# Performance work log

Measured on AMD Instinct MI355X. Metric: run time of the kernel, lower is better.

The kernel has to match this reference:

```python
import jax, jax.numpy as jnp
import numpy as np

L, B, P, D, H, DH, KV, M, S, A = 12, 8, 800, 1024, 8, 256, 1, 4096, 50, 32
ROPE_BASE = 10000.0
NEG = -1e30


def _rms(x, w):
    return (x * jax.lax.rsqrt(jnp.mean(x * x, -1, keepdims=True) + 1e-6)) * (1.0 + w)


def _rope(x, cos, sin):
    # x: [B,h,S,DH]; cos/sin: [B,1,S,DH//2]
    x1, x2 = jnp.split(x, 2, axis=-1)
    return jnp.concatenate([x1 * cos - x2 * sin, x2 * cos + x1 * sin], -1)


def setup_inputs() -> dict:
    key = jax.random.key(0)
    ks = iter(jax.random.split(key, 40))
    def nrm(shape, s=0.02):
        return jax.random.normal(next(ks), shape, jnp.float32) * s
    return {
        'prefix_pad_masks': jnp.ones((B, P), jnp.bool_),
        'x_t': jax.random.normal(next(ks), (B, S, A), jnp.float32),
        'timestep': jax.random.uniform(next(ks), (B,), jnp.float32),
        'dt': jnp.full((1,), 0.1, jnp.float32),
        'cache_k': nrm((L, B, KV, P, DH), 1.0),
        'cache_v': nrm((L, B, KV, P, DH), 1.0),
        'w_act_in': nrm((A, D)), 'b_act_in': jnp.zeros((D,), jnp.float32),
        'w_t1': nrm((D, D)), 'b_t1': jnp.zeros((D,), jnp.float32),
        'w_t2': nrm((D, D)), 'b_t2': jnp.zeros((D,), jnp.float32),
        'ln1_w': jnp.zeros((L, D), jnp.float32),
        'ada1_w': nrm((L, D, D)),
        'ln2_w': jnp.zeros((L, D), jnp.float32),
        'wq': nrm((L, D, H * DH)), 'wk': nrm((L, D, KV * DH)),
        'wv': nrm((L, D, KV * DH)), 'wo': nrm((L, H * DH, D)),
        'wg': nrm((L, D, M)), 'wu': nrm((L, D, M)), 'wd': nrm((L, M, D)),
        'lnf_w': jnp.zeros((D,), jnp.float32), 'adaf_w': nrm((D, D)),
        'w_act_out': nrm((D, A)), 'b_act_out': jnp.zeros((A,), jnp.float32),
    }


def reference(prefix_pad_masks, x_t, timestep, dt, cache_k, cache_v,
              w_act_in, b_act_in, w_t1, b_t1, w_t2, b_t2,
              ln1_w, ada1_w, ln2_w, wq, wk, wv, wo, wg, wu, wd,
              lnf_w, adaf_w, w_act_out, b_act_out):
    b, s, _ = x_t.shape
    p = prefix_pad_masks.shape[1]
    # --- embed_suffix: action projection + sinusoidal time -> MLP -> adaRMS cond ---
    suffix = x_t @ w_act_in + b_act_in                              # [B,S,D]
    half = D // 2
    freqs = jnp.exp(-jnp.log(jnp.float32(10000.0)) * jnp.arange(half, dtype=jnp.float32) / half)
    ang = timestep[:, None] * freqs[None, :]
    temb = jnp.concatenate([jnp.sin(ang), jnp.cos(ang)], -1)        # [B,D]
    cond = jax.nn.silu(temb @ w_t1 + b_t1) @ w_t2 + b_t2            # adarms_cond [B,D]
    # --- prefix-suffix 2D attention mask (make_att_2d_masks_trt) ---
    suffix_pad = jnp.ones((b, s), jnp.int32)
    suffix_att = jnp.concatenate([jnp.ones((b, 1), jnp.int32), jnp.zeros((b, s - 1), jnp.int32)], 1)
    cums = jnp.cumsum(suffix_att, 1)
    att2d = cums[:, None, :] <= cums[:, :, None]
    pad2d = (suffix_pad[:, None, :] * suffix_pad[:, :, None]).astype(bool)
    pre2d = jnp.broadcast_to(prefix_pad_masks[:, None, :], (b, s, p))
    full = jnp.concatenate([pre2d, att2d & pad2d], 2)               # [B,S,P+S]
    bias = jnp.where(full, 0.0, NEG)[:, None, :, :].astype(jnp.float32)
    # --- position ids: prefix offset + suffix cumsum - 1 ---
    offs = jnp.sum(prefix_pad_masks.astype(jnp.int32), -1)[:, None]
    pos = offs + jnp.cumsum(suffix_pad, 1) - 1                      # [B,S]
    inv = 1.0 / (ROPE_BASE ** (jnp.arange(0, DH, 2, dtype=jnp.float32) / DH))
    rang = pos[..., None].astype(jnp.float32) * inv                 # [B,S,DH/2]
    cos = jnp.cos(rang)[:, None]
    sin = jnp.sin(rang)[:, None]
    # --- gemma expert (eager attention over KV cache + suffix) ---
    h = suffix * jnp.sqrt(jnp.float32(D))
    def layer(hc, xs):
        l1, a1, l2, Wq, Wk, Wv, Wo, Wg, Wu, Wd, ck, cv = xs
        x = _rms(hc, l1) * (1.0 + (cond @ a1)[:, None, :])
        q = (x @ Wq).reshape(b, s, H, DH).transpose(0, 2, 1, 3)
        k = (x @ Wk).reshape(b, s, KV, DH).transpose(0, 2, 1, 3)
        v = (x @ Wv).reshape(b, s, KV, DH).transpose(0, 2, 1, 3)
        q = _rope(q, cos, sin)
        k = _rope(k, cos, sin)
        kf = jnp.repeat(jnp.concatenate([ck, k], 2), H // KV, 1)    # [B,H,P+S,DH]
        vf = jnp.repeat(jnp.concatenate([cv, v], 2), H // KV, 1)
        sc = jnp.einsum('bhsd,bhtd->bhst', q, kf) / jnp.sqrt(jnp.float32(DH)) + bias
        at = jax.nn.softmax(sc, -1)
        o = jnp.einsum('bhst,bhtd->bhsd', at, vf).transpose(0, 2, 1, 3).reshape(b, s, H * DH)
        hc = hc + o @ Wo
        x2 = _rms(hc, l2)
        hc = hc + (jax.nn.gelu(x2 @ Wg, approximate=True) * (x2 @ Wu)) @ Wd
        return hc, None
    h, _ = jax.lax.scan(layer, h, (ln1_w, ada1_w, ln2_w, wq, wk, wv, wo, wg, wu, wd, cache_k, cache_v))
    hf = _rms(h, lnf_w) * (1.0 + (cond @ adaf_w)[:, None, :])
    v_t = hf[:, -S:].astype(jnp.float32) @ w_act_out + b_act_out    # action_out_proj
    return x_t + dt.reshape(1, 1, 1) * v_t                          # Euler step
```

## Files before the change

kernel.cpp:

```cpp
#include <hip/hip_runtime.h>
#include <hip/hip_bf16.h>
#include <math.h>

#define NLAYER 12
#define NB 8
#define NP 800
#define ND 1024
#define NH 8
#define NDH 256
#define NM 4096
#define NS 50
#define NA 32
#define NKEYS 850
#define KPAD 896
#define CH 128

typedef unsigned short ushort_t;
typedef unsigned int u32;
using f32x4  = __attribute__((ext_vector_type(4))) float;
using short8 = __attribute__((ext_vector_type(8))) short;

__device__ __forceinline__ u32 pack_bf2(float lo, float hi) {
  u32 a = __float_as_uint(lo);
  u32 b = __float_as_uint(hi);
  a += 0x7fffu + ((a >> 16) & 1u);
  b += 0x7fffu + ((b >> 16) & 1u);
  return (a >> 16) | (b & 0xffff0000u);
}
__device__ __forceinline__ ushort_t bf1(float x) {
  u32 a = __float_as_uint(x);
  a += 0x7fffu + ((a >> 16) & 1u);
  return (ushort_t)(a >> 16);
}
__device__ __forceinline__ float ubf(ushort_t h) {
  return __uint_as_float(((u32)h) << 16);
}
__device__ __forceinline__ void async_cp16(const void* g, const void* l) {
  __builtin_amdgcn_global_load_lds(
      (const __attribute__((address_space(1))) u32*)g,
      (__attribute__((address_space(3))) u32*)l, 16, 0, 0);
}


__global__ void cvt_permute_kernel(const float* __restrict__ src, ushort_t* __restrict__ dst, long nrows) {
  long idx = (long)blockIdx.x * 256 + threadIdx.x;
  long row = idx >> 5;
  int t = (int)(idx & 31);
  if (row >= nrows) return;
  const float* s = src + row * 256 + t * 4;
  float4 lo = *reinterpret_cast<const float4*>(s);
  float4 hi = *reinterpret_cast<const float4*>(s + 128);
  ushort_t* d = dst + row * 256 + t * 8;
  *reinterpret_cast<uint4*>(d) =
      make_uint4(pack_bf2(lo.x, hi.x), pack_bf2(lo.y, hi.y),
                 pack_bf2(lo.z, hi.z), pack_bf2(lo.w, hi.w));
}

template<int MODE>
__global__ __launch_bounds__(256) void transpose_cvt(
    const float* __restrict__ src, long sz, ushort_t* __restrict__ dst, long dz,
    int R, int C, int ldd, int halfOff) {
  __shared__ float Ls[64][65];
  const float* s = src + (long)blockIdx.z * sz;
  ushort_t* d    = dst + (long)blockIdx.z * dz;
  int c0 = blockIdx.x * 64, r0 = blockIdx.y * 64;
  int t = threadIdx.x;
  int rr = t >> 4;
  int cc = (t & 15) * 4;
#pragma unroll
  for (int j = 0; j < 4; ++j) {
    int rl = rr + j * 16;
    int r = r0 + rl;
    float4 v = make_float4(0.f, 0.f, 0.f, 0.f);
    if (r < R) v = *reinterpret_cast<const float4*>(s + (long)r * C + c0 + cc);
    Ls[rl][cc] = v.x; Ls[rl][cc+1] = v.y; Ls[rl][cc+2] = v.z; Ls[rl][cc+3] = v.w;
  }
  __syncthreads();
  int dr = t >> 2;
  int rc = (t & 3) * 16;
  int cg = c0 + dr;
  long orow;
  if (MODE == 0)      orow = cg;
  else if (MODE == 1) orow = ((long)(cg >> 5) << 6) + (cg & 31) + halfOff;
  else                orow = (long)(cg & ~255) + ((cg & 127) << 1) + ((cg >> 7) & 1);
  ushort_t* drow = d + orow * ldd + r0 + rc;
#pragma unroll
  for (int i = 0; i < 16; i += 2) {
    int sr = r0 + rc + i;
    if (sr < R) {
      u32 p = pack_bf2(Ls[rc + i][dr], Ls[rc + i + 1][dr]);
      *reinterpret_cast<u32*>(drow + i) = p;
    }
  }
}


__global__ void temb_kernel(const float* __restrict__ ts, float* __restrict__ temb) {
  int idx = blockIdx.x * 256 + threadIdx.x;
  if (idx >= NB * ND) return;
  int b = idx >> 10, d = idx & 1023;
  int i = d & 511;
  float f = __expf(-logf(10000.f) * (float)i / 512.f);
  float ang = ts[b] * f;
  temb[idx] = (d < 512) ? sinf(ang) : cosf(ang);
}

__global__ void suffix_kernel(const float* __restrict__ x_t, const float* __restrict__ w,
                              const float* __restrict__ bias, float* __restrict__ h) {
  int m = blockIdx.x;
  __shared__ float xs[NA];
  if (threadIdx.x < NA) xs[threadIdx.x] = x_t[m * NA + threadIdx.x];
  __syncthreads();
  for (int n = threadIdx.x; n < ND; n += 256) {
    float acc = bias[n];
#pragma unroll
    for (int k = 0; k < NA; ++k) acc += xs[k] * w[k * ND + n];
    h[m * ND + n] = acc * 32.0f;
  }
}

__global__ void rope_table_kernel(float* __restrict__ cosT, float* __restrict__ sinT) {
  int idx = blockIdx.x * 256 + threadIdx.x;
  if (idx >= NS * 128) return;
  int s = idx >> 7, i = idx & 127;
  float inv = __expf(-(float)(2 * i) / 256.f * logf(10000.f));
  float ang = (float)(NP + s) * inv;
  cosT[idx] = cosf(ang);
  sinT[idx] = sinf(ang);
}

template<bool BFOUT>
__global__ void rms_kernel(const float* __restrict__ hin, const float* __restrict__ w,
                           const float* __restrict__ ada, void* __restrict__ outv) {
  int m = blockIdx.x;
  int b = m / NS;
  int d0 = threadIdx.x * 4;
  float4 v = *reinterpret_cast<const float4*>(hin + (long)m * ND + d0);
  float ss = v.x*v.x + v.y*v.y + v.z*v.z + v.w*v.w;
#pragma unroll
  for (int off = 32; off > 0; off >>= 1) ss += __shfl_down(ss, off);
  __shared__ float red[4];
  int lane = threadIdx.x & 63, wid = threadIdx.x >> 6;
  if (lane == 0) red[wid] = ss;
  __syncthreads();
  float tot = red[0] + red[1] + red[2] + red[3];
  float r = rsqrtf(tot * (1.f / ND) + 1e-6f);
  float4 wv = *reinterpret_cast<const float4*>(w + d0);
  float4 o;
  o.x = v.x * r * (1.f + wv.x);
  o.y = v.y * r * (1.f + wv.y);
  o.z = v.z * r * (1.f + wv.z);
  o.w = v.w * r * (1.f + wv.w);
  if (ada) {
    float4 av = *reinterpret_cast<const float4*>(ada + (long)b * ND + d0);
    o.x *= (1.f + av.x); o.y *= (1.f + av.y); o.z *= (1.f + av.z); o.w *= (1.f + av.w);
  }
  if (BFOUT) {
    *reinterpret_cast<uint2*>((ushort_t*)outv + (long)m * ND + d0) =
        make_uint2(pack_bf2(o.x, o.y), pack_bf2(o.z, o.w));
  } else {
    *reinterpret_cast<float4*>((float*)outv + (long)m * ND + d0) = o;
  }
}

__global__ void final_kernel(const float* __restrict__ hf, const float* __restrict__ w,
                             const float* __restrict__ bias, const float* __restrict__ x_t,
                             const float* __restrict__ dt, float* __restrict__ out) {
  int m = blockIdx.x;
  int a = threadIdx.x & 31;
  int kg = threadIdx.x >> 5;
  float acc = 0.f;
  for (int k = kg; k < ND; k += 8) acc += hf[(long)m * ND + k] * w[k * NA + a];
  __shared__ float red[256];
  red[threadIdx.x] = acc;
  __syncthreads();
  if (threadIdx.x < NA) {
    float s = 0.f;
#pragma unroll
    for (int g = 0; g < 8; ++g) s += red[g * 32 + a];
    out[m * NA + a] = x_t[m * NA + a] + dt[0] * (s + bias[a]);
  }
}

__global__ __launch_bounds__(256) void gemm64acc(
    const ushort_t* __restrict__ A,
    const ushort_t* __restrict__ B,
    float* __restrict__ C,
    int M, int N, int K, int lda, int ldb, int ldc, int kpb) {
  const int kbeg = blockIdx.z * kpb;
  const int kend = kbeg + kpb;

  const int m0 = blockIdx.x * 64;
  const int n0 = blockIdx.y * 64;
  const int tid = threadIdx.x;
  const int lane = tid & 63;
  const int wbase = tid & 192;
  const int wid = wbase >> 6;
  const int wm = (wid >> 1) * 32;
  const int wn = (wid & 1) * 32;
  const int l15 = lane & 15;
  const int l4  = lane >> 4;

  __shared__ ushort_t As[2][64 * 64];
  __shared__ ushort_t Bs[2][64 * 64];

  f32x4 acc[2][2] = {};

  const int ci0 = wbase + lane;
  const int row0 = ci0 >> 3;
  const int kc0 = (ci0 & 7) << 3;
  const int ci1 = 256 + ci0;
  const int row1 = ci1 >> 3;
  const int kc1 = (ci1 & 7) << 3;
  int gra0 = m0 + row0; if (gra0 > M - 1) gra0 = M - 1;
  int gra1 = m0 + row1; if (gra1 > M - 1) gra1 = M - 1;
  const int n_0 = n0 + row0;
  const int n_1 = n0 + row1;

  auto stage = [&](int buf, int k0) {
    async_cp16(A + (long)gra0 * lda + k0 + kc0, (const char*)As[buf] + ci0 * 16);
    async_cp16(B + (long)n_0 * ldb + k0 + kc0, (const char*)Bs[buf] + ci0 * 16);
    async_cp16(A + (long)gra1 * lda + k0 + kc1, (const char*)As[buf] + ci1 * 16);
    async_cp16(B + (long)n_1 * ldb + k0 + kc1, (const char*)Bs[buf] + ci1 * 16);
  };

  const int nt = (kend - kbeg) >> 6;
  stage(0, kbeg);
  __syncthreads();
  int cur = 0;
  for (int t = 0; t < nt; ++t) {
    if (t + 1 < nt) stage(cur ^ 1, kbeg + (t + 1) * 64);
    const ushort_t* Ac = As[cur];
    const ushort_t* Bc = Bs[cur];
#pragma unroll
    for (int ks = 0; ks < 2; ++ks) {
      short8 af[2], bf[2];
#pragma unroll
      for (int mi = 0; mi < 2; ++mi)
        af[mi] = *reinterpret_cast<const short8*>(&Ac[(wm + mi * 16 + l15) * 64 + ks * 32 + l4 * 8]);
#pragma unroll
      for (int ni = 0; ni < 2; ++ni)
        bf[ni] = *reinterpret_cast<const short8*>(&Bc[(wn + ni * 16 + l15) * 64 + ks * 32 + l4 * 8]);
#pragma unroll
      for (int mi = 0; mi < 2; ++mi)
#pragma unroll
        for (int ni = 0; ni < 2; ++ni)
          acc[mi][ni] = __builtin_amdgcn_mfma_f32_16x16x32_bf16(af[mi], bf[ni], acc[mi][ni], 0, 0, 0);
    }
    __syncthreads();
    cur ^= 1;
  }

#pragma unroll
  for (int mi = 0; mi < 2; ++mi) {
#pragma unroll
    for (int ni = 0; ni < 2; ++ni) {
      int col = n0 + wn + ni * 16 + l15;
      int rb  = m0 + wm + mi * 16 + l4 * 4;
      if (col >= N) continue;
#pragma unroll
      for (int r = 0; r < 4; ++r) {
        int row = rb + r;
        if (row >= M) continue;
        atomicAdd(&C[(long)row * ldc + col], acc[mi][ni][r]);
      }
    }
  }
}

__global__ __launch_bounds__(256) void gemm64rope(
    const ushort_t* __restrict__ A,
    const ushort_t* __restrict__ B,
    const float* __restrict__ cosT, const float* __restrict__ sinT,
    ushort_t* __restrict__ qTo, ushort_t* __restrict__ k_new,
    ushort_t* __restrict__ vT_l) {
  const int M = 400, K = 1024, lda = 1024, ldb = 1024;
  const int m0 = blockIdx.x * 64;
  const int n0 = blockIdx.y * 64;
  const int tid = threadIdx.x;
  const int lane = tid & 63;
  const int wbase = tid & 192;
  const int wid = wbase >> 6;
  const int wm = (wid >> 1) * 32;
  const int wn = (wid & 1) * 32;
  const int l15 = lane & 15;
  const int l4  = lane >> 4;

  __shared__ ushort_t As[2][64 * 64];
  __shared__ ushort_t Bs[2][64 * 64];

  f32x4 acc[2][2] = {};

  const int ci0 = wbase + lane;
  const int row0 = ci0 >> 3;
  const int kc0 = (ci0 & 7) << 3;
  const int ci1 = 256 + ci0;
  const int row1 = ci1 >> 3;
  const int kc1 = (ci1 & 7) << 3;
  int gra0 = m0 + row0; if (gra0 > M - 1) gra0 = M - 1;
  int gra1 = m0 + row1; if (gra1 > M - 1) gra1 = M - 1;
  const int n_0 = n0 + row0;
  const int n_1 = n0 + row1;

  auto stage = [&](int buf, int k0) {
    async_cp16(A + (long)gra0 * lda + k0 + kc0, (const char*)As[buf] + ci0 * 16);
    async_cp16(B + (long)n_0 * ldb + k0 + kc0, (const char*)Bs[buf] + ci0 * 16);
    async_cp16(A + (long)gra1 * lda + k0 + kc1, (const char*)As[buf] + ci1 * 16);
    async_cp16(B + (long)n_1 * ldb + k0 + kc1, (const char*)Bs[buf] + ci1 * 16);
  };

  stage(0, 0);
  __syncthreads();
  int cur = 0;
  for (int t = 0; t < 16; ++t) {
    if (t + 1 < 16) stage(cur ^ 1, (t + 1) * 64);
    const ushort_t* Ac = As[cur];
    const ushort_t* Bc = Bs[cur];
#pragma unroll
    for (int ks = 0; ks < 2; ++ks) {
      short8 af[2], bf[2];
#pragma unroll
      for (int mi = 0; mi < 2; ++mi)
        af[mi] = *reinterpret_cast<const short8*>(&Ac[(wm + mi * 16 + l15) * 64 + ks * 32 + l4 * 8]);
#pragma unroll
      for (int ni = 0; ni < 2; ++ni)
        bf[ni] = *reinterpret_cast<const short8*>(&Bc[(wn + ni * 16 + l15) * 64 + ks * 32 + l4 * 8]);
#pragma unroll
      for (int mi = 0; mi < 2; ++mi)
#pragma unroll
        for (int ni = 0; ni < 2; ++ni)
          acc[mi][ni] = __builtin_amdgcn_mfma_f32_16x16x32_bf16(af[mi], bf[ni], acc[mi][ni], 0, 0, 0);
    }
    __syncthreads();
    cur ^= 1;
  }

#pragma unroll
  for (int mi = 0; mi < 2; ++mi) {
#pragma unroll
    for (int ni = 0; ni < 2; ++ni) {
      int col = n0 + wn + ni * 16 + l15;
      int rb  = m0 + wm + mi * 16 + l4 * 4;
      float pv[4];
#pragma unroll
      for (int r = 0; r < 4; ++r) pv[r] = __shfl_xor(acc[mi][ni][r], 1);
#pragma unroll
      for (int r = 0; r < 4; ++r) {
        int row = rb + r;
        if (row >= 400) continue;
        int b = row / NS, s = row - b * NS;
        float v = acc[mi][ni][r];
        if (col < 2304) {
          int j = col & 255;
          int i = j >> 1;
          float c = cosT[s * 128 + i], sn = sinT[s * 128 + i];
          float o = (col & 1) ? (v * c + pv[r] * sn) : (v * c - pv[r] * sn);
          if (col < 2048)
            qTo[((long)((b << 3) + (col >> 8)) * NS + s) * 256 + j] = bf1(o);
          else
            k_new[(long)row * 256 + j] = bf1(o);
        } else {
          vT_l[((long)(b * 256 + (col - 2304))) * KPAD + NP + s] = bf1(v);
        }
      }
    }
  }
}

__global__ __launch_bounds__(256) void flash_kernel(
    const ushort_t* __restrict__ qT,
    const ushort_t* __restrict__ kcache_l,
    const ushort_t* __restrict__ k_new,
    const ushort_t* __restrict__ vT_l,
    const ushort_t* __restrict__ zpad,
    float* __restrict__ opart, float* __restrict__ mpart, float* __restrict__ lpart) {
  const int bh = blockIdx.x;
  const int ch = blockIdx.y;
  const int b  = bh >> 3;
  const int tid = threadIdx.x;
  const int lane = tid & 63;
  const int w = tid >> 6;
  const int wm = (w >> 1) * 32;
  const int wns = (w & 1) * 64;
  const int l15 = lane & 15;
  const int l4  = lane >> 4;

  __shared__ __align__(16) char lds[66560];
  ushort_t* Qs = (ushort_t*)lds;
  ushort_t* Ks = (ushort_t*)(lds + 32768);
  ushort_t* Ps = (ushort_t*)(lds + 49152);
  float* SMm = (float*)(lds + 65536);
  float* SMl = (float*)(lds + 66048);
  ushort_t* Vs = (ushort_t*)lds;

#pragma unroll
  for (int i = 0; i < 8; ++i) {
    int ci = i * 256 + tid;
    int qrow = ci >> 5; int seg = ci & 31;
    int qr = qrow < NS ? qrow : NS - 1;
    async_cp16(qT + ((long)bh * NS + qr) * 256 + seg * 8, (char*)Qs + ci * 16);
  }

  f32x4 s2[2][4] = {};
  for (int kk = 0; kk < 4; ++kk) {
#pragma unroll
    for (int i = 0; i < 4; ++i) {
      int ci = i * 256 + tid;
      int krow = ci >> 3; int seg = ci & 7;
      int key = ch * CH + krow;
      const ushort_t* src;
      if (key < NP)         src = kcache_l + ((long)(b * NP + key)) * 256 + kk * 64 + seg * 8;
      else if (key < NKEYS) src = k_new + ((long)(b * NS + key - NP)) * 256 + kk * 64 + seg * 8;
      else                  src = zpad + seg * 8;
      async_cp16(src, (char*)Ks + ci * 16);
    }
    __syncthreads();
#pragma unroll
    for (int ks = 0; ks < 2; ++ks) {
      short8 af[2], bf[4];
#pragma unroll
      for (int mi = 0; mi < 2; ++mi)
        af[mi] = *reinterpret_cast<const short8*>(&Qs[(wm + mi * 16 + l15) * 256 + kk * 64 + ks * 32 + l4 * 8]);
#pragma unroll
      for (int ni = 0; ni < 4; ++ni)
        bf[ni] = *reinterpret_cast<const short8*>(&Ks[(wns + ni * 16 + l15) * 64 + ks * 32 + l4 * 8]);
#pragma unroll
      for (int mi = 0; mi < 2; ++mi)
#pragma unroll
        for (int ni = 0; ni < 4; ++ni)
          s2[mi][ni] = __builtin_amdgcn_mfma_f32_16x16x32_bf16(af[mi], bf[ni], s2[mi][ni], 0, 0, 0);
    }
    __syncthreads();
  }

  float mx[2][4];
#pragma unroll
  for (int mi = 0; mi < 2; ++mi)
#pragma unroll
    for (int r = 0; r < 4; ++r) mx[mi][r] = -1e30f;
#pragma unroll
  for (int mi = 0; mi < 2; ++mi)
#pragma unroll
    for (int ni = 0; ni < 4; ++ni) {
      int key = ch * CH + wns + ni * 16 + l15;
      bool valid = key < NKEYS;
#pragma unroll
      for (int r = 0; r < 4; ++r) {
        float v = s2[mi][ni][r] * 0.0625f;
        v = valid ? v : -1e30f;
        s2[mi][ni][r] = v;
        mx[mi][r] = fmaxf(mx[mi][r], v);
      }
    }
#pragma unroll
  for (int off = 1; off < 16; off <<= 1)
#pragma unroll
    for (int mi = 0; mi < 2; ++mi)
#pragma unroll
      for (int r = 0; r < 4; ++r)
        mx[mi][r] = fmaxf(mx[mi][r], __shfl_xor(mx[mi][r], off));
  if (l15 == 0) {
#pragma unroll
    for (int mi = 0; mi < 2; ++mi)
#pragma unroll
      for (int r = 0; r < 4; ++r)
        SMm[(w & 1) * 64 + wm + mi * 16 + l4 * 4 + r] = mx[mi][r];
  }
  __syncthreads();
  float mrow[2][4], sum[2][4];
#pragma unroll
  for (int mi = 0; mi < 2; ++mi)
#pragma unroll
    for (int r = 0; r < 4; ++r) {
      int row = wm + mi * 16 + l4 * 4 + r;
      mrow[mi][r] = fmaxf(SMm[row], SMm[64 + row]);
      sum[mi][r] = 0.f;
    }
#pragma unroll
  for (int mi = 0; mi < 2; ++mi)
#pragma unroll
    for (int ni = 0; ni < 4; ++ni) {
      int colp = wns + ni * 16 + l15;
#pragma unroll
      for (int r = 0; r < 4; ++r) {
        float e = __expf(s2[mi][ni][r] - mrow[mi][r]);
        Ps[(wm + mi * 16 + l4 * 4 + r) * 128 + colp] = bf1(e);
        sum[mi][r] += e;
      }
    }
#pragma unroll
  for (int off = 1; off < 16; off <<= 1)
#pragma unroll
    for (int mi = 0; mi < 2; ++mi)
#pragma unroll
      for (int r = 0; r < 4; ++r)
        sum[mi][r] += __shfl_xor(sum[mi][r], off);
  if (l15 == 0) {
#pragma unroll
    for (int mi = 0; mi < 2; ++mi)
#pragma unroll
      for (int r = 0; r < 4; ++r)
        SMl[(w & 1) * 64 + wm + mi * 16 + l4 * 4 + r] = sum[mi][r];
  }
  __syncthreads();
  if ((w & 1) == 0 && l15 == 0) {
#pragma unroll
    for (int mi = 0; mi < 2; ++mi)
#pragma unroll
      for (int r = 0; r < 4; ++r) {
        int row = wm + mi * 16 + l4 * 4 + r;
        if (row < NS) {
          mpart[((long)bh * 7 + ch) * NS + row] = mrow[mi][r];
          lpart[((long)bh * 7 + ch) * NS + row] = SMl[row] + SMl[64 + row];
        }
      }
  }

  f32x4 o2[2][8] = {};
  for (int kk = 0; kk < 2; ++kk) {
#pragma unroll
    for (int i = 0; i < 8; ++i) {
      int ci = i * 256 + tid;
      int vd = ci >> 3; int seg = ci & 7;
      async_cp16(vT_l + ((long)(b * 256 + vd)) * KPAD + ch * CH + kk * 64 + seg * 8,
                 (char*)Vs + ci * 16);
    }
    __syncthreads();
#pragma unroll
    for (int ks = 0; ks < 2; ++ks) {
      short8 af[2], bf[8];
#pragma unroll
      for (int mi = 0; mi < 2; ++mi)
        af[mi] = *reinterpret_cast<const short8*>(&Ps[(wm + mi * 16 + l15) * 128 + kk * 64 + ks * 32 + l4 * 8]);
#pragma unroll
      for (int ni = 0; ni < 8; ++ni)
        bf[ni] = *reinterpret_cast<const short8*>(&Vs[((w & 1) * 128 + ni * 16 + l15) * 64 + ks * 32 + l4 * 8]);
#pragma unroll
      for (int mi = 0; mi < 2; ++mi)
#pragma unroll
        for (int ni = 0; ni < 8; ++ni)
          o2[mi][ni] = __builtin_amdgcn_mfma_f32_16x16x32_bf16(af[mi], bf[ni], o2[mi][ni], 0, 0, 0);
    }
    __syncthreads();
  }

#pragma unroll
  for (int mi = 0; mi < 2; ++mi)
#pragma unroll
    for (int ni = 0; ni < 8; ++ni) {
      int col = (w & 1) * 128 + ni * 16 + l15;
#pragma unroll
      for (int r = 0; r < 4; ++r) {
        int row = wm + mi * 16 + l4 * 4 + r;
        if (row < NS)
          opart[(((long)bh * 7 + ch) * NS + row) * 256 + col] = o2[mi][ni][r];
      }
    }
}

__global__ void att_combine(const float* __restrict__ opart, const float* __restrict__ mpart,
                            const float* __restrict__ lpart, ushort_t* __restrict__ o_buf) {
  int blk = blockIdx.x;
  int b = blk / NS, s = blk - b * NS;
  int d = threadIdx.x;
  for (int h = 0; h < NH; ++h) {
    int bh = b * NH + h;
    float mv[7];
    float m = -1e30f;
#pragma unroll
    for (int c = 0; c < 7; ++c) {
      mv[c] = mpart[((long)bh * 7 + c) * NS + s];
      m = fmaxf(m, mv[c]);
    }
    float den = 0.f, o = 0.f;
#pragma unroll
    for (int c = 0; c < 7; ++c) {
      float wgt = __expf(mv[c] - m);
      den += wgt * lpart[((long)bh * 7 + c) * NS + s];
      o   += wgt * opart[(((long)bh * 7 + c) * NS + s) * 256 + d];
    }
    o_buf[(long)blk * 2048 + h * 256 + d] = bf1(o / den);
  }
}

__global__ __launch_bounds__(256) void gemm64G(
    const ushort_t* __restrict__ A, const ushort_t* __restrict__ B,
    ushort_t* __restrict__ C, int M, int K, int lda, int ldb, int ldc) {
  const int m0 = blockIdx.x * 64;
  const int n0 = blockIdx.y * 64;
  const int tid = threadIdx.x;
  const int lane = tid & 63;
  const int wbase = tid & 192;
  const int wid = wbase >> 6;
  const int l15 = lane & 15;
  const int l4  = lane >> 4;

  __shared__ ushort_t As[2][64 * 64];
  __shared__ ushort_t Bs[2][64 * 64];

  f32x4 acc[4] = {};

  const int ci0 = wbase + lane;
  const int row0 = ci0 >> 3;
  const int kc0 = (ci0 & 7) << 3;
  const int ci1 = 256 + ci0;
  const int row1 = ci1 >> 3;
  const int kc1 = (ci1 & 7) << 3;
  int gra0 = m0 + row0; if (gra0 > M - 1) gra0 = M - 1;
  int gra1 = m0 + row1; if (gra1 > M - 1) gra1 = M - 1;

  auto stage = [&](int buf, int k0) {
    async_cp16(A + (long)gra0 * lda + k0 + kc0, (const char*)As[buf] + ci0 * 16);
    async_cp16(B + (long)(n0 + row0) * ldb + k0 + kc0, (const char*)Bs[buf] + ci0 * 16);
    async_cp16(A + (long)gra1 * lda + k0 + kc1, (const char*)As[buf] + ci1 * 16);
    async_cp16(B + (long)(n0 + row1) * ldb + k0 + kc1, (const char*)Bs[buf] + ci1 * 16);
  };

  const int nt = K >> 6;
  stage(0, 0);
  __syncthreads();
  int cur = 0;
  for (int t = 0; t < nt; ++t) {
    if (t + 1 < nt) stage(cur ^ 1, (t + 1) * 64);
    const ushort_t* Ac = As[cur];
    const ushort_t* Bc = Bs[cur];
#pragma unroll
    for (int ks = 0; ks < 2; ++ks) {
      short8 af = *reinterpret_cast<const short8*>(&Ac[(wid * 16 + l15) * 64 + ks * 32 + l4 * 8]);
#pragma unroll
      for (int ni = 0; ni < 4; ++ni) {
        short8 bf = *reinterpret_cast<const short8*>(&Bc[(ni * 16 + l15) * 64 + ks * 32 + l4 * 8]);
        acc[ni] = __builtin_amdgcn_mfma_f32_16x16x32_bf16(af, bf, acc[ni], 0, 0, 0);
      }
    }
    __syncthreads();
    cur ^= 1;
  }

#pragma unroll
  for (int ni = 0; ni < 2; ++ni) {
    int col = (n0 >> 1) + ni * 16 + l15;
    int rb  = m0 + wid * 16 + l4 * 4;
#pragma unroll
    for (int r = 0; r < 4; ++r) {
      int row = rb + r;
      if (row >= M) continue;
      float g = acc[ni][r];
      float u = acc[ni + 2][r];
      float inner = 0.7978845608028654f * (g + 0.044715f * g * g * g);
      float t = 0.5f * g * (1.f + tanhf(inner));
      C[(long)row * ldc + col] = bf1(t * u);
    }
  }
}

template<int EPI>
__global__ __launch_bounds__(256)
void gemm_f32_kernel(const float* __restrict__ A,
                     const float* __restrict__ B1,
                     float* __restrict__ C,
                     int M, int N, int K, int lda, int ldb, int ldc,
                     const float* __restrict__ bias) {
  const int m0 = blockIdx.x * 64;
  const int n0 = blockIdx.y * 64;
  const int tid = threadIdx.x;
  const int lane = tid & 63;
  const int wid = tid >> 6;
  const int wm = (wid >> 1) * 32;
  const int wn = (wid & 1) * 32;
  const int l15 = lane & 15;
  const int l4  = lane >> 4;

  __shared__ __align__(16) ushort_t As[64][72];
  __shared__ __align__(16) ushort_t Bs[64][72];

  f32x4 acc[2][2] = {};

  for (int k0 = 0; k0 < K; k0 += 64) {
#pragma unroll
    for (int pass = 0; pass < 2; ++pass) {
      int c = tid + pass * 256;
      int row = c >> 3;
      int kc = (c & 7) * 8;
      int gr = m0 + row, gk = k0 + kc;
      float v[8];
#pragma unroll
      for (int j = 0; j < 8; ++j)
        v[j] = (gr < M && gk + j < K) ? A[(long)gr * lda + gk + j] : 0.f;
      *reinterpret_cast<uint4*>(&As[row][kc]) =
          make_uint4(pack_bf2(v[0],v[1]), pack_bf2(v[2],v[3]),
                     pack_bf2(v[4],v[5]), pack_bf2(v[6],v[7]));
    }
    {
      int n = tid & 63;
      int kg = tid >> 6;
      int gn = n0 + n;
      u32 pk[8];
#pragma unroll
      for (int kk = 0; kk < 16; kk += 2) {
        int kga = k0 + kg * 16 + kk;
        float v0 = (gn < N && kga < K)     ? B1[(long)kga * ldb + gn] : 0.f;
        float v1 = (gn < N && kga + 1 < K) ? B1[(long)(kga + 1) * ldb + gn] : 0.f;
        pk[kk >> 1] = pack_bf2(v0, v1);
      }
      *reinterpret_cast<uint4*>(&Bs[n][kg * 16])     = make_uint4(pk[0],pk[1],pk[2],pk[3]);
      *reinterpret_cast<uint4*>(&Bs[n][kg * 16 + 8]) = make_uint4(pk[4],pk[5],pk[6],pk[7]);
    }
    __syncthreads();
#pragma unroll
    for (int ks = 0; ks < 2; ++ks) {
      short8 af[2], bfr[2];
#pragma unroll
      for (int mi = 0; mi < 2; ++mi)
        af[mi] = *reinterpret_cast<const short8*>(&As[wm + mi*16 + l15][ks*32 + l4*8]);
#pragma unroll
      for (int ni = 0; ni < 2; ++ni)
        bfr[ni] = *reinterpret_cast<const short8*>(&Bs[wn + ni*16 + l15][ks*32 + l4*8]);
#pragma unroll
      for (int mi = 0; mi < 2; ++mi)
#pragma unroll
        for (int ni = 0; ni < 2; ++ni)
          acc[mi][ni] = __builtin_amdgcn_mfma_f32_16x16x32_bf16(af[mi], bfr[ni], acc[mi][ni], 0, 0, 0);
    }
    __syncthreads();
  }

#pragma unroll
  for (int mi = 0; mi < 2; ++mi) {
#pragma unroll
    for (int ni = 0; ni < 2; ++ni) {
      int col = n0 + wn + ni * 16 + l15;
      int rb  = m0 + wm + mi * 16 + l4 * 4;
#pragma unroll
      for (int r = 0; r < 4; ++r) {
        int row = rb + r;
        if (row < M && col < N) {
          float v = acc[mi][ni][r];
          if (EPI == 1) C[(long)row * ldc + col] = v + bias[col];
          else {
            float t = v + bias[col];
            C[(long)row * ldc + col] = t / (1.f + __expf(-t));
          }
        }
      }
    }
  }
}

__global__ __launch_bounds__(256)
void gemm_f32sk(const float* __restrict__ A,
                const float* __restrict__ B, long bz,
                float* __restrict__ C, long cz,
                int M, int N, int K, int lda, int ldb, int ldc, int nks) {
  const int zz = blockIdx.z;
  const int layer = zz / nks;
  const int chunk = zz % nks;
  const int kpb = K / nks;
  const int kbeg = chunk * kpb, kend = kbeg + kpb;
  const float* Bb = B + (long)layer * bz;
  float* Cb = C + (long)layer * cz;

  const int m0 = blockIdx.x * 64;
  const int n0 = blockIdx.y * 64;
  const int tid = threadIdx.x;
  const int lane = tid & 63;
  const int wid = tid >> 6;
  const int wm = (wid >> 1) * 32;
  const int wn = (wid & 1) * 32;
  const int l15 = lane & 15;
  const int l4  = lane >> 4;

  __shared__ __align__(16) ushort_t As[64][72];
  __shared__ __align__(16) ushort_t Bs[64][72];

  f32x4 acc[2][2] = {};

  for (int k0 = kbeg; k0 < kend; k0 += 64) {
#pragma unroll
    for (int pass = 0; pass < 2; ++pass) {
      int c = tid + pass * 256;
      int row = c >> 3;
      int kc = (c & 7) * 8;
      int gr = m0 + row, gk = k0 + kc;
      float v[8];
#pragma unroll
      for (int j = 0; j < 8; ++j)
        v[j] = (gr < M) ? A[(long)gr * lda + gk + j] : 0.f;
      *reinterpret_cast<uint4*>(&As[row][kc]) =
          make_uint4(pack_bf2(v[0],v[1]), pack_bf2(v[2],v[3]),
                     pack_bf2(v[4],v[5]), pack_bf2(v[6],v[7]));
    }
    {
      int n = tid & 63;
      int kg = tid >> 6;
      int gn = n0 + n;
      u32 pk[8];
#pragma unroll
      for (int kk = 0; kk < 16; kk += 2) {
        int kga = k0 + kg * 16 + kk;
        float v0 = Bb[(long)kga * ldb + gn];
        float v1 = Bb[(long)(kga + 1) * ldb + gn];
        pk[kk >> 1] = pack_bf2(v0, v1);
      }
      *reinterpret_cast<uint4*>(&Bs[n][kg * 16])     = make_uint4(pk[0],pk[1],pk[2],pk[3]);
      *reinterpret_cast<uint4*>(&Bs[n][kg * 16 + 8]) = make_uint4(pk[4],pk[5],pk[6],pk[7]);
    }
    __syncthreads();
#pragma unroll
    for (int ks = 0; ks < 2; ++ks) {
      short8 af[2], bfr[2];
#pragma unroll
      for (int mi = 0; mi < 2; ++mi)
        af[mi] = *reinterpret_cast<const short8*>(&As[wm + mi*16 + l15][ks*32 + l4*8]);
#pragma unroll
      for (int ni = 0; ni < 2; ++ni)
        bfr[ni] = *reinterpret_cast<const short8*>(&Bs[wn + ni*16 + l15][ks*32 + l4*8]);
#pragma unroll
      for (int mi = 0; mi < 2; ++mi)
#pragma unroll
        for (int ni = 0; ni < 2; ++ni)
          acc[mi][ni] = __builtin_amdgcn_mfma_f32_16x16x32_bf16(af[mi], bfr[ni], acc[mi][ni], 0, 0, 0);
    }
    __syncthreads();
  }

#pragma unroll
  for (int mi = 0; mi < 2; ++mi) {
#pragma unroll
    for (int ni = 0; ni < 2; ++ni) {
      int col = n0 + wn + ni * 16 + l15;
      int rb  = m0 + wm + mi * 16 + l4 * 4;
#pragma unroll
      for (int r = 0; r < 4; ++r) {
        int row = rb + r;
        if (row < M && col < N)
          atomicAdd(&Cb[(long)row * ldc + col], acc[mi][ni][r]);
      }
    }
  }
}

extern "C" void kernel_launch(void* const* d_in, const int* in_sizes, int n_in,
                              void* d_out, int out_size, void* d_ws, size_t ws_size,
                              hipStream_t stream) {
  (void)in_sizes; (void)n_in; (void)out_size; (void)ws_size;
  const float* x_t      = (const float*)d_in[1];
  const float* tstep    = (const float*)d_in[2];
  const float* dtp      = (const float*)d_in[3];
  const float* cache_k  = (const float*)d_in[4];
  const float* cache_v  = (const float*)d_in[5];
  const float* w_act_in = (const float*)d_in[6];
  const float* b_act_in = (const float*)d_in[7];
  const float* w_t1     = (const float*)d_in[8];
  const float* b_t1     = (const float*)d_in[9];
  const float* w_t2     = (const float*)d_in[10];
  const float* b_t2     = (const float*)d_in[11];
  const float* ln1_w    = (const float*)d_in[12];
  const float* ada1_w   = (const float*)d_in[13];
  const float* ln2_w    = (const float*)d_in[14];
  const float* wq       = (const float*)d_in[15];
  const float* wk       = (const float*)d_in[16];
  const float* wv       = (const float*)d_in[17];
  const float* wo       = (const float*)d_in[18];
  const float* wg       = (const float*)d_in[19];
  const float* wu       = (const float*)d_in[20];
  const float* wd       = (const float*)d_in[21];
  const float* lnf_w    = (const float*)d_in[22];
  const float* adaf_w   = (const float*)d_in[23];
  const float* wao      = (const float*)d_in[24];
  const float* bao      = (const float*)d_in[25];
  float* outp = (float*)d_out;

  char* p = (char*)d_ws;
  auto alloc = [&](size_t bytes) { char* r = p; p += (bytes + 255) & ~(size_t)255; return r; };

  ushort_t* wqkvT  = (ushort_t*)alloc((size_t)12 * 2560 * 1024 * 2);
  ushort_t* woT    = (ushort_t*)alloc((size_t)12 * 1024 * 2048 * 2);
  ushort_t* wguT   = (ushort_t*)alloc((size_t)12 * 8192 * 1024 * 2);
  ushort_t* wdT    = (ushort_t*)alloc((size_t)12 * 1024 * 4096 * 2);
  ushort_t* kcache = (ushort_t*)alloc((size_t)12 * 8 * NP * 256 * 2);
  ushort_t* vT     = (ushort_t*)alloc((size_t)12 * 8 * 256 * KPAD * 2);
  ushort_t* qT     = (ushort_t*)alloc((size_t)64 * NS * 256 * 2);
  ushort_t* k_new  = (ushort_t*)alloc((size_t)400 * 256 * 2);
  float*    opart  = (float*)alloc((size_t)64 * 7 * NS * 256 * 4);
  float*    mpart  = (float*)alloc((size_t)64 * 7 * NS * 4);
  float*    lpart  = (float*)alloc((size_t)64 * 7 * NS * 4);
  ushort_t* o_buf  = (ushort_t*)alloc((size_t)400 * 2048 * 2);
  ushort_t* t_buf  = (ushort_t*)alloc((size_t)400 * 4096 * 2);
  ushort_t* x_buf  = (ushort_t*)alloc((size_t)400 * 1024 * 2);
  float*    h_buf  = (float*)alloc((size_t)400 * 1024 * 4);
  float*    hf     = (float*)alloc((size_t)400 * 1024 * 4);
  float*    temb   = (float*)alloc(8 * 1024 * 4);
  float*    tmp    = (float*)alloc(8 * 1024 * 4);
  float*    cond   = (float*)alloc(8 * 1024 * 4);
  float*    ada_all= (float*)alloc((size_t)12 * 8 * 1024 * 4);
  float*    adaf_o = (float*)alloc(8 * 1024 * 4);
  float*    cosT   = (float*)alloc(NS * 128 * 4);
  float*    sinT   = (float*)alloc(NS * 128 * 4);
  ushort_t* zpad   = (ushort_t*)alloc(512 * 2);

  hipMemsetAsync(zpad, 0, 512 * 2, stream);
  hipMemsetAsync(ada_all, 0, ((size_t)12 * 8 * 1024 + 8 * 1024) * 4, stream);

  cvt_permute_kernel<<<9600, 256, 0, stream>>>(cache_k, kcache, (long)12 * 8 * NP);
  transpose_cvt<2><<<dim3(32, 16, 12), 256, 0, stream>>>(wq, (long)1024 * 2048, wqkvT, (long)2560 * 1024, 1024, 2048, 1024, 0);
  transpose_cvt<2><<<dim3(4, 16, 12), 256, 0, stream>>>(wk, (long)1024 * 256, wqkvT + (long)2048 * 1024, (long)2560 * 1024, 1024, 256, 1024, 0);
  transpose_cvt<0><<<dim3(4, 16, 12), 256, 0, stream>>>(wv, (long)1024 * 256, wqkvT + (long)2304 * 1024, (long)2560 * 1024, 1024, 256, 1024, 0);
  transpose_cvt<0><<<dim3(16, 32, 12), 256, 0, stream>>>(wo, (long)2048 * 1024, woT, (long)1024 * 2048, 2048, 1024, 2048, 0);
  transpose_cvt<1><<<dim3(64, 16, 12), 256, 0, stream>>>(wg, (long)1024 * 4096, wguT, (long)8192 * 1024, 1024, 4096, 1024, 0);
  transpose_cvt<1><<<dim3(64, 16, 12), 256, 0, stream>>>(wu, (long)1024 * 4096, wguT, (long)8192 * 1024, 1024, 4096, 1024, 32);
  transpose_cvt<0><<<dim3(16, 64, 12), 256, 0, stream>>>(wd, (long)4096 * 1024, wdT, (long)1024 * 4096, 4096, 1024, 4096, 0);
  transpose_cvt<0><<<dim3(4, 13, 96), 256, 0, stream>>>(cache_v, (long)NP * 256, vT, (long)256 * KPAD, NP, 256, KPAD, 0);

  temb_kernel<<<32, 256, 0, stream>>>(tstep, temb);
  suffix_kernel<<<400, 256, 0, stream>>>(x_t, w_act_in, b_act_in, h_buf);
  rope_table_kernel<<<25, 256, 0, stream>>>(cosT, sinT);
  gemm_f32_kernel<2><<<dim3(1, 16, 1), 256, 0, stream>>>(temb, w_t1, tmp, NB, ND, ND, ND, ND, ND, b_t1);
  gemm_f32_kernel<1><<<dim3(1, 16, 1), 256, 0, stream>>>(tmp, w_t2, cond, NB, ND, ND, ND, ND, ND, b_t2);
  gemm_f32sk<<<dim3(1, 16, 48), 256, 0, stream>>>(cond, ada1_w, (long)ND * ND, ada_all, (long)NB * ND, NB, ND, ND, ND, ND, ND, 4);
  gemm_f32sk<<<dim3(1, 16, 4), 256, 0, stream>>>(cond, adaf_w, 0, adaf_o, 0, NB, ND, ND, ND, ND, ND, 4);

  for (int l = 0; l < NLAYER; ++l) {
    ushort_t* vT_l = vT + (long)l * 8 * 256 * KPAD;
    rms_kernel<true><<<400, 256, 0, stream>>>(h_buf, ln1_w + (long)l * ND, ada_all + (long)l * NB * ND, x_buf);
    gemm64rope<<<dim3(7, 40, 1), 256, 0, stream>>>(
        x_buf, wqkvT + (long)l * 2560 * 1024, cosT, sinT, qT, k_new, vT_l);
    flash_kernel<<<dim3(64, 7, 1), 256, 0, stream>>>(
        qT, kcache + (long)l * 8 * NP * 256, k_new, vT_l, zpad, opart, mpart, lpart);
    att_combine<<<400, 256, 0, stream>>>(opart, mpart, lpart, o_buf);
    gemm64acc<<<dim3(7, 16, 4), 256, 0, stream>>>(
        o_buf, woT + (long)l * 1024 * 2048, h_buf, 400, 1024, 2048, 2048, 2048, 1024, 512);
    rms_kernel<true><<<400, 256, 0, stream>>>(h_buf, ln2_w + (long)l * ND, nullptr, x_buf);
    gemm64G<<<dim3(7, 128, 1), 256, 0, stream>>>(
        x_buf, wguT + (long)l * 8192 * 1024, t_buf, 400, 1024, 1024, 1024, 4096);
    gemm64acc<<<dim3(7, 16, 4), 256, 0, stream>>>(
        t_buf, wdT + (long)l * 1024 * 4096, h_buf, 400, 1024, 4096, 4096, 4096, 1024, 1024);
  }

  rms_kernel<false><<<400, 256, 0, stream>>>(h_buf, lnf_w, adaf_o, hf);
  final_kernel<<<400, 256, 0, stream>>>(hf, wao, bao, x_t, dtp, outp);
}
```

Baseline: 2.042 ms.

## Restructure flash attention into 256-key chunks with double-buffered K/V staging

```diff
diff --git a/kernel.cpp b/kernel.cpp
--- a/kernel.cpp
+++ b/kernel.cpp
@@ -12,8 +12,7 @@
 #define NS 50
 #define NA 32
 #define NKEYS 850
-#define KPAD 896
-#define CH 128
+#define KPAD 1024
 
 typedef unsigned short ushort_t;
 typedef unsigned int u32;
@@ -163,15 +162,36 @@
   }
 }
 
-__global__ void final_kernel(const float* __restrict__ hf, const float* __restrict__ w,
-                             const float* __restrict__ bias, const float* __restrict__ x_t,
-                             const float* __restrict__ dt, float* __restrict__ out) {
+__global__ void final_fused(const float* __restrict__ hin, const float* __restrict__ lnf,
+                            const float* __restrict__ adaf, const float* __restrict__ w,
+                            const float* __restrict__ bias, const float* __restrict__ x_t,
+                            const float* __restrict__ dt, float* __restrict__ out) {
   int m = blockIdx.x;
+  int b = m / NS;
+  int d0 = threadIdx.x * 4;
+  __shared__ float hfs[ND];
+  __shared__ float red[256];
+  float4 v = *reinterpret_cast<const float4*>(hin + (long)m * ND + d0);
+  float ss = v.x*v.x + v.y*v.y + v.z*v.z + v.w*v.w;
+#pragma unroll
+  for (int off = 32; off > 0; off >>= 1) ss += __shfl_down(ss, off);
+  __shared__ float red4[4];
+  int lane = threadIdx.x & 63, wid = threadIdx.x >> 6;
+  if (lane == 0) red4[wid] = ss;
+  __syncthreads();
+  float tot = red4[0] + red4[1] + red4[2] + red4[3];
+  float r = rsqrtf(tot * (1.f / ND) + 1e-6f);
+  float4 wv = *reinterpret_cast<const float4*>(lnf + d0);
+  float4 av = *reinterpret_cast<const float4*>(adaf + (long)b * ND + d0);
+  hfs[d0]     = v.x * r * (1.f + wv.x) * (1.f + av.x);
+  hfs[d0 + 1] = v.y * r * (1.f + wv.y) * (1.f + av.y);
+  hfs[d0 + 2] = v.z * r * (1.f + wv.z) * (1.f + av.z);
+  hfs[d0 + 3] = v.w * r * (1.f + wv.w) * (1.f + av.w);
+  __syncthreads();
   int a = threadIdx.x & 31;
   int kg = threadIdx.x >> 5;
   float acc = 0.f;
-  for (int k = kg; k < ND; k += 8) acc += hf[(long)m * ND + k] * w[k * NA + a];
-  __shared__ float red[256];
+  for (int k = kg; k < ND; k += 8) acc += hfs[k] * w[k * NA + a];
   red[threadIdx.x] = acc;
   __syncthreads();
   if (threadIdx.x < NA) {
@@ -274,7 +294,7 @@
     const float* __restrict__ cosT, const float* __restrict__ sinT,
     ushort_t* __restrict__ qTo, ushort_t* __restrict__ k_new,
     ushort_t* __restrict__ vT_l) {
-  const int M = 400, K = 1024, lda = 1024, ldb = 1024;
+  const int M = 400, lda = 1024, ldb = 1024;
   const int m0 = blockIdx.x * 64;
   const int n0 = blockIdx.y * 64;
   const int tid = threadIdx.x;
@@ -367,7 +387,7 @@
   }
 }
 
-__global__ __launch_bounds__(256) void flash_kernel(
+__global__ __launch_bounds__(256) void flash2_kernel(
     const ushort_t* __restrict__ qT,
     const ushort_t* __restrict__ kcache_l,
     const ushort_t* __restrict__ k_new,
@@ -381,57 +401,83 @@
   const int lane = tid & 63;
   const int w = tid >> 6;
   const int wm = (w >> 1) * 32;
-  const int wns = (w & 1) * 64;
+  const int wn = (w & 1) * 128;
   const int l15 = lane & 15;
   const int l4  = lane >> 4;
 
-  __shared__ __align__(16) char lds[66560];
-  ushort_t* Qs = (ushort_t*)lds;
-  ushort_t* Ks = (ushort_t*)(lds + 32768);
-  ushort_t* Ps = (ushort_t*)(lds + 49152);
-  float* SMm = (float*)(lds + 65536);
-  float* SMl = (float*)(lds + 66048);
-  ushort_t* Vs = (ushort_t*)lds;
-
-#pragma unroll
-  for (int i = 0; i < 8; ++i) {
-    int ci = i * 256 + tid;
-    int qrow = ci >> 5; int seg = ci & 31;
-    int qr = qrow < NS ? qrow : NS - 1;
-    async_cp16(qT + ((long)bh * NS + qr) * 256 + seg * 8, (char*)Qs + ci * 16);
-  }
-
-  f32x4 s2[2][4] = {};
-  for (int kk = 0; kk < 4; ++kk) {
-#pragma unroll
-    for (int i = 0; i < 4; ++i) {
+  __shared__ __align__(16) char lds[100352];
+  ushort_t* KV0 = (ushort_t*)lds;
+  ushort_t* KV1 = (ushort_t*)(lds + 32768);
+  ushort_t* Ps  = (ushort_t*)(lds + 65536);
+  float* SMm = (float*)(lds + 99328);
+  float* SMl = (float*)(lds + 99840);
+
+  short8 qf[4][2][2];
+  {
+    const ushort_t* qbase = qT + (long)bh * NS * 256;
+#pragma unroll
+    for (int mi = 0; mi < 2; ++mi) {
+      int row = wm + mi * 16 + l15;
+      int qr = row < NS ? row : NS - 1;
+      const ushort_t* qrow = qbase + (long)qr * 256;
+#pragma unroll
+      for (int s = 0; s < 4; ++s)
+#pragma unroll
+        for (int ks = 0; ks < 2; ++ks)
+          qf[s][mi][ks] = *reinterpret_cast<const short8*>(qrow + s * 64 + ks * 32 + l4 * 8);
+    }
+  }
+
+  auto stageK = [&](ushort_t* buf, int s) {
+#pragma unroll
+    for (int i = 0; i < 8; ++i) {
       int ci = i * 256 + tid;
-      int krow = ci >> 3; int seg = ci & 7;
-      int key = ch * CH + krow;
+      int key = ch * 256 + (ci >> 3);
+      int seg = ci & 7;
       const ushort_t* src;
-      if (key < NP)         src = kcache_l + ((long)(b * NP + key)) * 256 + kk * 64 + seg * 8;
-      else if (key < NKEYS) src = k_new + ((long)(b * NS + key - NP)) * 256 + kk * 64 + seg * 8;
+      if (key < NP)         src = kcache_l + ((long)(b * NP + key)) * 256 + s * 64 + seg * 8;
+      else if (key < NKEYS) src = k_new + ((long)(b * NS + key - NP)) * 256 + s * 64 + seg * 8;
       else                  src = zpad + seg * 8;
-      async_cp16(src, (char*)Ks + ci * 16);
-    }
+      async_cp16(src, (char*)buf + ci * 16);
+    }
+  };
+  auto stageV = [&](ushort_t* buf, int s) {
+#pragma unroll
+    for (int i = 0; i < 8; ++i) {
+      int ci = i * 256 + tid;
+      int dout = ci >> 3;
+      int seg = ci & 7;
+      async_cp16(vT_l + ((long)(b * 256 + dout)) * KPAD + ch * 256 + s * 64 + seg * 8,
+                 (char*)buf + ci * 16);
+    }
+  };
+
+  f32x4 s2[2][8] = {};
+  stageK(KV0, 0);
+  __syncthreads();
+#pragma unroll
+  for (int s = 0; s < 4; ++s) {
+    ushort_t* buf = (s & 1) ? KV1 : KV0;
+    ushort_t* nxt = (s & 1) ? KV0 : KV1;
+    if (s < 3) stageK(nxt, s + 1);
+    __builtin_amdgcn_s_setprio(1);
+#pragma unroll
+    for (int ks = 0; ks < 2; ++ks) {
+      short8 bf[8];
+#pragma unroll
+      for (int ni = 0; ni < 8; ++ni)
+        bf[ni] = *reinterpret_cast<const short8*>(&buf[(wn + ni * 16 + l15) * 64 + ks * 32 + l4 * 8]);
+#pragma unroll
+      for (int mi = 0; mi < 2; ++mi)
+#pragma unroll
+        for (int ni = 0; ni < 8; ++ni)
+          s2[mi][ni] = __builtin_amdgcn_mfma_f32_16x16x32_bf16(qf[s][mi][ks], bf[ni], s2[mi][ni], 0, 0, 0);
+    }
+    __builtin_amdgcn_s_setprio(0);
     __syncthreads();
-#pragma unroll
-    for (int ks = 0; ks < 2; ++ks) {
-      short8 af[2], bf[4];
-#pragma unroll
-      for (int mi = 0; mi < 2; ++mi)
-        af[mi] = *reinterpret_cast<const short8*>(&Qs[(wm + mi * 16 + l15) * 256 + kk * 64 + ks * 32 + l4 * 8]);
-#pragma unroll
-      for (int ni = 0; ni < 4; ++ni)
-        bf[ni] = *reinterpret_cast<const short8*>(&Ks[(wns + ni * 16 + l15) * 64 + ks * 32 + l4 * 8]);
-#pragma unroll
-      for (int mi = 0; mi < 2; ++mi)
-#pragma unroll
-        for (int ni = 0; ni < 4; ++ni)
-          s2[mi][ni] = __builtin_amdgcn_mfma_f32_16x16x32_bf16(af[mi], bf[ni], s2[mi][ni], 0, 0, 0);
-    }
-    __syncthreads();
-  }
+  }
+
+  stageV(KV0, 0);
 
   float mx[2][4];
 #pragma unroll
@@ -441,8 +487,8 @@
 #pragma unroll
   for (int mi = 0; mi < 2; ++mi)
 #pragma unroll
-    for (int ni = 0; ni < 4; ++ni) {
-      int key = ch * CH + wns + ni * 16 + l15;
+    for (int ni = 0; ni < 8; ++ni) {
+      int key = ch * 256 + wn + ni * 16 + l15;
       bool valid = key < NKEYS;
 #pragma unroll
       for (int r = 0; r < 4; ++r) {
@@ -479,12 +525,12 @@
 #pragma unroll
   for (int mi = 0; mi < 2; ++mi)
 #pragma unroll
-    for (int ni = 0; ni < 4; ++ni) {
-      int colp = wns + ni * 16 + l15;
+    for (int ni = 0; ni < 8; ++ni) {
+      int colp = wn + ni * 16 + l15;
 #pragma unroll
       for (int r = 0; r < 4; ++r) {
         float e = __expf(s2[mi][ni][r] - mrow[mi][r]);
-        Ps[(wm + mi * 16 + l4 * 4 + r) * 128 + colp] = bf1(e);
+        Ps[(wm + mi * 16 + l4 * 4 + r) * 264 + colp] = bf1(e);
         sum[mi][r] += e;
       }
     }
@@ -510,37 +556,35 @@
       for (int r = 0; r < 4; ++r) {
         int row = wm + mi * 16 + l4 * 4 + r;
         if (row < NS) {
-          mpart[((long)bh * 7 + ch) * NS + row] = mrow[mi][r];
-          lpart[((long)bh * 7 + ch) * NS + row] = SMl[row] + SMl[64 + row];
+          mpart[((long)bh * 4 + ch) * NS + row] = mrow[mi][r];
+          lpart[((long)bh * 4 + ch) * NS + row] = SMl[row] + SMl[64 + row];
         }
       }
   }
 
   f32x4 o2[2][8] = {};
-  for (int kk = 0; kk < 2; ++kk) {
-#pragma unroll
-    for (int i = 0; i < 8; ++i) {
-      int ci = i * 256 + tid;
-      int vd = ci >> 3; int seg = ci & 7;
-      async_cp16(vT_l + ((long)(b * 256 + vd)) * KPAD + ch * CH + kk * 64 + seg * 8,
-                 (char*)Vs + ci * 16);
-    }
-    __syncthreads();
+#pragma unroll
+  for (int s = 0; s < 4; ++s) {
+    ushort_t* buf = (s & 1) ? KV1 : KV0;
+    ushort_t* nxt = (s & 1) ? KV0 : KV1;
+    if (s < 3) stageV(nxt, s + 1);
+    __builtin_amdgcn_s_setprio(1);
 #pragma unroll
     for (int ks = 0; ks < 2; ++ks) {
       short8 af[2], bf[8];
 #pragma unroll
       for (int mi = 0; mi < 2; ++mi)
-        af[mi] = *reinterpret_cast<const short8*>(&Ps[(wm + mi * 16 + l15) * 128 + kk * 64 + ks * 32 + l4 * 8]);
+        af[mi] = *reinterpret_cast<const short8*>(&Ps[(wm + mi * 16 + l15) * 264 + s * 64 + ks * 32 + l4 * 8]);
 #pragma unroll
       for (int ni = 0; ni < 8; ++ni)
-        bf[ni] = *reinterpret_cast<const short8*>(&Vs[((w & 1) * 128 + ni * 16 + l15) * 64 + ks * 32 + l4 * 8]);
+        bf[ni] = *reinterpret_cast<const short8*>(&buf[(wn + ni * 16 + l15) * 64 + ks * 32 + l4 * 8]);
 #pragma unroll
       for (int mi = 0; mi < 2; ++mi)
 #pragma unroll
         for (int ni = 0; ni < 8; ++ni)
           o2[mi][ni] = __builtin_amdgcn_mfma_f32_16x16x32_bf16(af[mi], bf[ni], o2[mi][ni], 0, 0, 0);
     }
+    __builtin_amdgcn_s_setprio(0);
     __syncthreads();
   }
 
@@ -548,12 +592,12 @@
   for (int mi = 0; mi < 2; ++mi)
 #pragma unroll
     for (int ni = 0; ni < 8; ++ni) {
-      int col = (w & 1) * 128 + ni * 16 + l15;
+      int col = wn + ni * 16 + l15;
 #pragma unroll
       for (int r = 0; r < 4; ++r) {
         int row = wm + mi * 16 + l4 * 4 + r;
         if (row < NS)
-          opart[(((long)bh * 7 + ch) * NS + row) * 256 + col] = o2[mi][ni][r];
+          opart[(((long)bh * 4 + ch) * NS + row) * 256 + col] = o2[mi][ni][r];
       }
     }
 }
@@ -565,19 +609,19 @@
   int d = threadIdx.x;
   for (int h = 0; h < NH; ++h) {
     int bh = b * NH + h;
-    float mv[7];
+    float mv[4];
     float m = -1e30f;
 #pragma unroll
-    for (int c = 0; c < 7; ++c) {
-      mv[c] = mpart[((long)bh * 7 + c) * NS + s];
+    for (int c = 0; c < 4; ++c) {
+      mv[c] = mpart[((long)bh * 4 + c) * NS + s];
       m = fmaxf(m, mv[c]);
     }
     float den = 0.f, o = 0.f;
 #pragma unroll
-    for (int c = 0; c < 7; ++c) {
+    for (int c = 0; c < 4; ++c) {
       float wgt = __expf(mv[c] - m);
-      den += wgt * lpart[((long)bh * 7 + c) * NS + s];
-      o   += wgt * opart[(((long)bh * 7 + c) * NS + s) * 256 + d];
+      den += wgt * lpart[((long)bh * 4 + c) * NS + s];
+      o   += wgt * opart[(((long)bh * 4 + c) * NS + s) * 256 + d];
     }
     o_buf[(long)blk * 2048 + h * 256 + d] = bf1(o / den);
   }
@@ -882,14 +926,13 @@
   ushort_t* vT     = (ushort_t*)alloc((size_t)12 * 8 * 256 * KPAD * 2);
   ushort_t* qT     = (ushort_t*)alloc((size_t)64 * NS * 256 * 2);
   ushort_t* k_new  = (ushort_t*)alloc((size_t)400 * 256 * 2);
-  float*    opart  = (float*)alloc((size_t)64 * 7 * NS * 256 * 4);
-  float*    mpart  = (float*)alloc((size_t)64 * 7 * NS * 4);
-  float*    lpart  = (float*)alloc((size_t)64 * 7 * NS * 4);
+  float*    opart  = (float*)alloc((size_t)64 * 4 * NS * 256 * 4);
+  float*    mpart  = (float*)alloc((size_t)64 * 4 * NS * 4);
+  float*    lpart  = (float*)alloc((size_t)64 * 4 * NS * 4);
   ushort_t* o_buf  = (ushort_t*)alloc((size_t)400 * 2048 * 2);
   ushort_t* t_buf  = (ushort_t*)alloc((size_t)400 * 4096 * 2);
   ushort_t* x_buf  = (ushort_t*)alloc((size_t)400 * 1024 * 2);
   float*    h_buf  = (float*)alloc((size_t)400 * 1024 * 4);
-  float*    hf     = (float*)alloc((size_t)400 * 1024 * 4);
   float*    temb   = (float*)alloc(8 * 1024 * 4);
   float*    tmp    = (float*)alloc(8 * 1024 * 4);
   float*    cond   = (float*)alloc(8 * 1024 * 4);
@@ -925,7 +968,7 @@
     rms_kernel<true><<<400, 256, 0, stream>>>(h_buf, ln1_w + (long)l * ND, ada_all + (long)l * NB * ND, x_buf);
     gemm64rope<<<dim3(7, 40, 1), 256, 0, stream>>>(
         x_buf, wqkvT + (long)l * 2560 * 1024, cosT, sinT, qT, k_new, vT_l);
-    flash_kernel<<<dim3(64, 7, 1), 256, 0, stream>>>(
+    flash2_kernel<<<dim3(64, 4, 1), 256, 0, stream>>>(
         qT, kcache + (long)l * 8 * NP * 256, k_new, vT_l, zpad, opart, mpart, lpart);
     att_combine<<<400, 256, 0, stream>>>(opart, mpart, lpart, o_buf);
     gemm64acc<<<dim3(7, 16, 4), 256, 0, stream>>>(
@@ -937,6 +980,5 @@
         t_buf, wdT + (long)l * 1024 * 4096, h_buf, 400, 1024, 4096, 4096, 4096, 1024, 1024);
   }
 
-  rms_kernel<false><<<400, 256, 0, stream>>>(h_buf, lnf_w, adaf_o, hf);
-  final_kernel<<<400, 256, 0, stream>>>(hf, wao, bao, x_t, dtp, outp);
-}
+  final_fused<<<400, 256, 0, stream>>>(h_buf, lnf_w, adaf_o, wao, bao, x_t, dtp, outp);
+}
```

Result: faster. 1.998 ms (-2.2%).
